# Kernel tuning notes

Hardware: AMD Instinct MI355X
Metric: run time of the kernel (lower is better)

The kernel has to match this reference:

```python
import jax, jax.numpy as jnp
import numpy as np


def setup_inputs() -> dict:
    key = jax.random.key(0)
    N, D = 131072, 128
    x = jax.random.normal(key, (N, D), dtype=jnp.float32)
    return {"x": x, "k": 1024, "niters": 10}


def reference(x, k, niters):
    """Lloyd's k-means, Euclidean metric. Returns (clusters, centroids, n_points).

    Matches torch semantics: clusters are the assignments computed at the START
    of the last iteration (against the previous centroids); centroids/n_points
    reflect the update performed in that last iteration. Empty clusters divide
    by zero (-> inf/nan), same as the torch code.
    """
    K = int(k)
    x_sq = jnp.sum(x * x, axis=-1)  # [N], constant across iterations
    c0 = x[:K]

    def step(centroids, _):
        d = (x_sq[:, None]
             - 2.0 * jnp.einsum('nd,kd->nk', x, centroids)
             + jnp.sum(centroids * centroids, axis=-1)[None, :])
        clusters = jnp.argmin(d, axis=1)  # [N] int32
        sums = jax.ops.segment_sum(x, clusters, num_segments=K)  # [K, D] scatter-add
        counts = jax.ops.segment_sum(jnp.ones((x.shape[0],), x.dtype), clusters,
                                     num_segments=K)  # [K] bincount
        new_centroids = sums / counts[:, None]
        return new_centroids, (clusters, counts)

    centroids, (clusters_hist, counts_hist) = jax.lax.scan(step, c0, None, length=int(niters))
    return clusters_hist[-1].astype(jnp.int64), centroids, counts_hist[-1]
```

## Files before the change

### kernel.cpp

```cpp
#include <hip/hip_runtime.h>
#include <math.h>

#define DIM 128
#define KC 1024
#define NITER 10
#define BM 128
#define NB 512
#define THRESH 0.01f

typedef __bf16 bf16x8 __attribute__((ext_vector_type(8)));
typedef float f32x4 __attribute__((ext_vector_type(4)));

__device__ __forceinline__ unsigned short bf16rne(float f) {
    unsigned int u = __float_as_uint(f);
    unsigned int r = (u + 0x7FFFu + ((u >> 16) & 1u)) >> 16;
    return (unsigned short)r;
}

__device__ __forceinline__ bf16x8 pack_hi8(const float* fv, unsigned short* hs) {
    bf16x8 out;
    #pragma unroll
    for (int e = 0; e < 8; e++) {
        unsigned short h = bf16rne(fv[e]);
        hs[e] = h;
        out[e] = __builtin_bit_cast(__bf16, h);
    }
    return out;
}

__device__ __forceinline__ float sq_np_row(const float* __restrict__ v) {
    const float4* row = (const float4*)v;
    float r[8];
    {
        float4 a = row[0], b = row[1];
        r[0] = __fmul_rn(a.x, a.x); r[1] = __fmul_rn(a.y, a.y);
        r[2] = __fmul_rn(a.z, a.z); r[3] = __fmul_rn(a.w, a.w);
        r[4] = __fmul_rn(b.x, b.x); r[5] = __fmul_rn(b.y, b.y);
        r[6] = __fmul_rn(b.z, b.z); r[7] = __fmul_rn(b.w, b.w);
    }
    #pragma unroll
    for (int blk = 1; blk < 16; blk++) {
        float4 a = row[blk * 2], b = row[blk * 2 + 1];
        r[0] = __fadd_rn(r[0], __fmul_rn(a.x, a.x));
        r[1] = __fadd_rn(r[1], __fmul_rn(a.y, a.y));
        r[2] = __fadd_rn(r[2], __fmul_rn(a.z, a.z));
        r[3] = __fadd_rn(r[3], __fmul_rn(a.w, a.w));
        r[4] = __fadd_rn(r[4], __fmul_rn(b.x, b.x));
        r[5] = __fadd_rn(r[5], __fmul_rn(b.y, b.y));
        r[6] = __fadd_rn(r[6], __fmul_rn(b.z, b.z));
        r[7] = __fadd_rn(r[7], __fmul_rn(b.w, b.w));
    }
    return __fadd_rn(__fadd_rn(__fadd_rn(r[0], r[1]), __fadd_rn(r[2], r[3])),
                     __fadd_rn(__fadd_rn(r[4], r[5]), __fadd_rn(r[6], r[7])));
}

__global__ void sq_np_kernel(const float* __restrict__ v, float* __restrict__ out, int rows) {
    int i = blockIdx.x * blockDim.x + threadIdx.x;
    if (i >= rows) return;
    out[i] = sq_np_row(v + (size_t)i * DIM);
}

__global__ __launch_bounds__(256, 3) void assign_mfma_kernel(
    const float* __restrict__ x,
    const ushort* __restrict__ centPh, const ushort* __restrict__ centPl,
    const float* __restrict__ csq,
    int* __restrict__ cl, int* __restrict__ fb_list, int* __restrict__ fbc)
{
    const int tid = threadIdx.x;
    const int lane = tid & 63;
    const int w = tid >> 6;
    const int bm = blockIdx.x * BM;
    const int row0 = bm + w * 32 + (lane & 15);
    const int ko = (lane >> 4) * 8;

    bf16x8 ah[2][4], al[2][4];
    #pragma unroll
    for (int m = 0; m < 2; m++) {
        const float* xr = x + (size_t)(row0 + m * 16) * DIM;
        #pragma unroll
        for (int dt = 0; dt < 4; dt++) {
            float4 a = *(const float4*)(xr + dt * 32 + ko);
            float4 b = *(const float4*)(xr + dt * 32 + ko + 4);
            float fv[8] = {a.x, a.y, a.z, a.w, b.x, b.y, b.z, b.w};
            unsigned short hs[8];
            ah[m][dt] = pack_hi8(fv, hs);
            bf16x8 lo;
            #pragma unroll
            for (int e = 0; e < 8; e++) {
                float rem = __fsub_rn(fv[e], __uint_as_float(((unsigned int)hs[e]) << 16));
                lo[e] = __builtin_bit_cast(__bf16, bf16rne(rem));
            }
            al[m][dt] = lo;
        }
    }

    float best1[8], best2[8];
    int bidx[8];
    int nanf = 0;
    #pragma unroll
    for (int s = 0; s < 8; s++) { best1[s] = INFINITY; best2[s] = INFINITY; bidx[s] = 0; }

    const ushort* pb = centPh + lane * 8;
    const ushort* qb = centPl + lane * 8;
    int kk = lane & 15;

    for (int kt = 0; kt < KC / 16; kt++) {
        const ushort* pk = pb + (size_t)kt * 2048;
        const ushort* qk = qb + (size_t)kt * 2048;
        bf16x8 bh0 = *(const bf16x8*)(pk);
        bf16x8 bh1 = *(const bf16x8*)(pk + 512);
        bf16x8 bh2 = *(const bf16x8*)(pk + 1024);
        bf16x8 bh3 = *(const bf16x8*)(pk + 1536);
        bf16x8 bl0 = *(const bf16x8*)(qk);
        bf16x8 bl1 = *(const bf16x8*)(qk + 512);
        bf16x8 bl2 = *(const bf16x8*)(qk + 1024);
        bf16x8 bl3 = *(const bf16x8*)(qk + 1536);

        f32x4 a0 = (f32x4){0.f, 0.f, 0.f, 0.f};
        f32x4 a1 = (f32x4){0.f, 0.f, 0.f, 0.f};
#define DT(BH, BL, D)                                                      \
        a0 = __builtin_amdgcn_mfma_f32_16x16x32_bf16(ah[0][D], BH, a0, 0, 0, 0); \
        a1 = __builtin_amdgcn_mfma_f32_16x16x32_bf16(ah[1][D], BH, a1, 0, 0, 0); \
        a0 = __builtin_amdgcn_mfma_f32_16x16x32_bf16(ah[0][D], BL, a0, 0, 0, 0); \
        a1 = __builtin_amdgcn_mfma_f32_16x16x32_bf16(ah[1][D], BL, a1, 0, 0, 0); \
        a0 = __builtin_amdgcn_mfma_f32_16x16x32_bf16(al[0][D], BH, a0, 0, 0, 0); \
        a1 = __builtin_amdgcn_mfma_f32_16x16x32_bf16(al[1][D], BH, a1, 0, 0, 0);
        DT(bh0, bl0, 0)
        DT(bh1, bl1, 1)
        DT(bh2, bl2, 2)
        DT(bh3, bl3, 3)
#undef DT

        float cq = csq[kk];
        nanf |= (cq != cq) ? 1 : 0;
        #pragma unroll
        for (int q = 0; q < 4; q++) {
            {
                float d = __fmaf_rn(-2.f, a0[q], cq);
                bool lt = (d < best1[q]);
                best2[q] = fminf(best2[q], lt ? best1[q] : d);
                if (lt) { best1[q] = d; bidx[q] = kk; }
            }
            {
                int s = 4 + q;
                float d = __fmaf_rn(-2.f, a1[q], cq);
                bool lt = (d < best1[s]);
                best2[s] = fminf(best2[s], lt ? best1[s] : d);
                if (lt) { best1[s] = d; bidx[s] = kk; }
            }
        }
        kk += 16;
    }

    #pragma unroll
    for (int mask = 1; mask < 16; mask <<= 1) {
        #pragma unroll
        for (int s = 0; s < 8; s++) {
            float ob1 = __shfl_xor(best1[s], mask, 64);
            float ob2 = __shfl_xor(best2[s], mask, 64);
            int   oi  = __shfl_xor(bidx[s],  mask, 64);
            float nb2 = fminf(fminf(best2[s], ob2), fmaxf(best1[s], ob1));
            bool take = (ob1 < best1[s]) || (ob1 == best1[s] && oi < bidx[s]);
            if (take) { best1[s] = ob1; bidx[s] = oi; }
            best2[s] = nb2;
        }
    }

    int wnan = __any(nanf);
    if ((lane & 15) == 0) {
        int hi = lane >> 4;
        #pragma unroll
        for (int s = 0; s < 8; s++) {
            int p = bm + w * 32 + (s >> 2) * 16 + hi * 4 + (s & 3);
            bool fb = (wnan != 0) || !(best2[s] - best1[s] > THRESH);
            if (fb) { int pos = atomicAdd(fbc, 1); fb_list[pos] = p; }
            else cl[p] = bidx[s];
        }
    }
}

__device__ __forceinline__ bool better(float od, int oi, float md, int mi) {
    bool n1 = (md != md), n2 = (od != od);
    if (n1 && n2) return oi < mi;
    if (n2) return true;
    if (n1) return false;
    return (od < md) || (od == md && oi < mi);
}

__global__ __launch_bounds__(256) void fixup_kernel(
    const float* __restrict__ x, const float* __restrict__ centTf,
    const float* __restrict__ xsq, const float* __restrict__ csq,
    const int* __restrict__ fb_list, const int* __restrict__ fbc,
    int* __restrict__ cl)
{
    __shared__ float xs[16][DIM];
    __shared__ float xqs[16];
    __shared__ int   ids[16];
    __shared__ float wv[16][4];
    __shared__ int   wi[16][4];
    const int t = threadIdx.x;
    const int lane = t & 63, wid = t >> 6;
    const int cnt = fbc[0];
    for (int w = blockIdx.x * 16; w < cnt; w += gridDim.x * 16) {
        int np = cnt - w; if (np > 16) np = 16;
        __syncthreads();
        if (t < np) { int i = fb_list[w + t]; ids[t] = i; xqs[t] = xsq[i]; }
        __syncthreads();
        for (int e = t; e < np * DIM; e += 256) {
            int p = e >> 7, d = e & 127;
            xs[p][d] = x[(size_t)ids[p] * DIM + d];
        }
        __syncthreads();
        float S[16][4];
        #pragma unroll
        for (int p = 0; p < 16; p++)
            #pragma unroll
            for (int c = 0; c < 4; c++) S[p][c] = 0.f;
        #pragma unroll 4
        for (int d = 0; d < DIM; d++) {
            const float* row = centTf + (size_t)d * KC;
            float c0 = row[t], c1 = row[t + 256], c2 = row[t + 512], c3 = row[t + 768];
            #pragma unroll
            for (int p = 0; p < 16; p++) {
                float xv = xs[p][d];
                S[p][0] = fmaf(xv, c0, S[p][0]);
                S[p][1] = fmaf(xv, c1, S[p][1]);
                S[p][2] = fmaf(xv, c2, S[p][2]);
                S[p][3] = fmaf(xv, c3, S[p][3]);
            }
        }
        float q0 = csq[t], q1 = csq[t + 256], q2 = csq[t + 512], q3 = csq[t + 768];
        #pragma unroll
        for (int p = 0; p < 16; p++) {
            float xq = xqs[p];
            float bb = INFINITY; int bi = 0x7fffffff;
            float dd; int c;
            c = t;       dd = __fadd_rn(__fsub_rn(xq, __fmul_rn(2.f, S[p][0])), q0); if (better(dd, c, bb, bi)) { bb = dd; bi = c; }
            c = t + 256; dd = __fadd_rn(__fsub_rn(xq, __fmul_rn(2.f, S[p][1])), q1); if (better(dd, c, bb, bi)) { bb = dd; bi = c; }
            c = t + 512; dd = __fadd_rn(__fsub_rn(xq, __fmul_rn(2.f, S[p][2])), q2); if (better(dd, c, bb, bi)) { bb = dd; bi = c; }
            c = t + 768; dd = __fadd_rn(__fsub_rn(xq, __fmul_rn(2.f, S[p][3])), q3); if (better(dd, c, bb, bi)) { bb = dd; bi = c; }
            #pragma unroll
            for (int mask = 1; mask < 64; mask <<= 1) {
                float od = __shfl_xor(bb, mask, 64);
                int   oi = __shfl_xor(bi, mask, 64);
                if (better(od, oi, bb, bi)) { bb = od; bi = oi; }
            }
            if (lane == 0) { wv[p][wid] = bb; wi[p][wid] = bi; }
        }
        __syncthreads();
        if (t < np) {
            float bb = wv[t][0]; int bi = wi[t][0];
            #pragma unroll
            for (int r = 1; r < 4; r++)
                if (better(wv[t][r], wi[t][r], bb, bi)) { bb = wv[t][r]; bi = wi[t][r]; }
            cl[ids[t]] = bi;
        }
    }
}


__global__ __launch_bounds__(256) void bhist_kernel(const int* __restrict__ cl,
                                                    int* __restrict__ bhist, int n,
                                                    int* __restrict__ fbc) {
    __shared__ int h[KC];
    int t = threadIdx.x;
    if (blockIdx.x == 0 && t == 0) { fbc[0] = 0; fbc[1] = 0; }
    #pragma unroll
    for (int q = 0; q < KC / 256; q++) h[t + q * 256] = 0;
    __syncthreads();
    int i = blockIdx.x * 256 + t;
    if (i < n) atomicAdd(&h[cl[i]], 1);
    __syncthreads();
    int* row = bhist + (size_t)blockIdx.x * KC;
    #pragma unroll
    for (int q = 0; q < KC / 256; q++) row[t + q * 256] = h[t + q * 256];
}

__global__ __launch_bounds__(256) void colsum_kernel(const int* __restrict__ bhist,
                                                     int* __restrict__ cnt) {
    int k = blockIdx.x * 256 + threadIdx.x;
    int s = 0;
    #pragma unroll 8
    for (int b = 0; b < NB; b++) s += bhist[(size_t)b * KC + k];
    cnt[k] = s;
}

__global__ __launch_bounds__(256) void blockpfx_kernel(int* __restrict__ bhist,
                                                       const int* __restrict__ cnt,
                                                       int* __restrict__ off) {
    __shared__ int lc[KC];
    __shared__ int ps[256];
    int t = threadIdx.x;
    int4 cv = *(const int4*)(cnt + t * 4);
    *(int4*)(lc + t * 4) = cv;
    ps[t] = cv.x + cv.y + cv.z + cv.w;
    __syncthreads();
    for (int o = 1; o < 256; o <<= 1) {
        int v = (t >= o) ? ps[t - o] : 0;
        __syncthreads();
        ps[t] += v;
        __syncthreads();
    }
    int k = blockIdx.x * 256 + t;
    int g = k >> 2;
    int run = (g > 0) ? ps[g - 1] : 0;
    for (int j = g * 4; j < k; j++) run += lc[j];
    off[k] = run;
    for (int b0 = 0; b0 < NB; b0 += 16) {
        int v[16];
        #pragma unroll
        for (int u = 0; u < 16; u++)
            v[u] = bhist[(size_t)(b0 + u) * KC + k];
        #pragma unroll
        for (int u = 0; u < 16; u++) {
            bhist[(size_t)(b0 + u) * KC + k] = run;
            run += v[u];
        }
    }
}

__global__ __launch_bounds__(256) void stable_scatter_kernel(
    const int* __restrict__ cl, const int* __restrict__ bhist,
    int* __restrict__ list, int n)
{
    __shared__ int cls[256];
    int t = threadIdx.x;
    int i = blockIdx.x * 256 + t;
    int c = (i < n) ? cl[i] : -1;
    cls[t] = c;
    __syncthreads();
    if (i >= n) return;
    int rank = 0;
    for (int j = 0; j < 256; j++)
        rank += (j < t && cls[j] == c) ? 1 : 0;
    list[bhist[(size_t)blockIdx.x * KC + c] + rank] = i;
}

#define CHUNK 512
__global__ __launch_bounds__(128) void sum_kernel(
    const float* __restrict__ x, const int* __restrict__ list,
    const int* __restrict__ off, const int* __restrict__ cnt,
    float* __restrict__ cent, ushort* __restrict__ centPh,
    ushort* __restrict__ centPl, float* __restrict__ centTf,
    float* __restrict__ csq, float* __restrict__ countsF)
{
    __attribute__((aligned(16))) __shared__ int sidx[CHUNK];
    int k = blockIdx.x;
    int d = threadIdx.x;
    int o = off[k], m = cnt[k];
    float s = 0.f;
    for (int base = 0; base < m; base += CHUNK) {
        int c = m - base; if (c > CHUNK) c = CHUNK;
        __syncthreads();
        for (int t = d; t < c; t += 128) sidx[t] = list[o + base + t];
        __syncthreads();
        int j = 0;
        for (; j + 16 <= c; j += 16) {
            float v[16];
            #pragma unroll
            for (int u = 0; u < 16; u++)
                v[u] = x[(size_t)sidx[j + u] * DIM + d];
            #pragma unroll
            for (int u = 0; u < 16; u++)
                s = __fadd_rn(s, v[u]);
        }
        for (; j < c; j++)
            s = __fadd_rn(s, x[(size_t)sidx[j] * DIM + d]);
    }
    float mv = __fdiv_rn(s, (float)m);
    cent[(size_t)k * DIM + d] = mv;
    centTf[(size_t)d * KC + k] = mv;
    unsigned short h = bf16rne(mv);
    unsigned short lo = bf16rne(__fsub_rn(mv, __uint_as_float(((unsigned int)h) << 16)));
    int pidx = (((k >> 4) * 4 + (d >> 5)) * 64 + ((k & 15) + 16 * ((d >> 3) & 3))) * 8 + (d & 7);
    centPh[pidx] = h;
    centPl[pidx] = lo;
    if (d == 0) countsF[k] = (float)m;
    __syncthreads();
    ((float*)sidx)[d] = mv;
    __syncthreads();
    if (d == 0) csq[k] = sq_np_row((const float*)sidx);
}

__global__ void init_centP_kernel(const float* __restrict__ x,
                                  ushort* __restrict__ centPh, ushort* __restrict__ centPl,
                                  float* __restrict__ centTf, int* __restrict__ fbc) {
    int i = blockIdx.x * 256 + threadIdx.x;
    if (i == 0) { fbc[0] = 0; fbc[1] = 0; }
    if (i < KC * DIM) {
        int k = i >> 7, d = i & 127;
        float v = x[i];
        centTf[(size_t)d * KC + k] = v;
        unsigned short h = bf16rne(v);
        unsigned short lo = bf16rne(__fsub_rn(v, __uint_as_float(((unsigned int)h) << 16)));
        int pidx = (((k >> 4) * 4 + (d >> 5)) * 64 + ((k & 15) + 16 * ((d >> 3) & 3))) * 8 + (d & 7);
        centPh[pidx] = h;
        centPl[pidx] = lo;
    }
}

__global__ void cl2f_kernel(const int* __restrict__ cl, float* __restrict__ out, int n) {
    int i = blockIdx.x * 256 + threadIdx.x;
    if (i < n) out[i] = (float)cl[i];
}

extern "C" void kernel_launch(void* const* d_in, const int* in_sizes, int n_in,
                              void* d_out, int out_size, void* d_ws, size_t ws_size,
                              hipStream_t stream) {
    const float* x = (const float*)d_in[0];
    const int n = in_sizes[0] / DIM;

    float* clf     = (float*)d_out;
    float* cent    = clf + n;
    float* countsF = cent + KC * DIM;

    float* xsq   = (float*)d_ws;
    float* csq   = xsq + n;
    int*   cl    = (int*)(csq + KC);
    int*   list  = cl + n;
    int*   cnt   = list + n;
    int*   off   = cnt + KC;
    int*   bhist = off + KC;
    ushort* centPh = (ushort*)(bhist + (size_t)NB * KC);
    ushort* centPl = centPh + KC * DIM;
    int*   fbc   = (int*)(centPl + KC * DIM);
    float* centTf = (float*)bhist;

    hipMemcpyAsync(cent, x, (size_t)KC * DIM * sizeof(float),
                   hipMemcpyDeviceToDevice, stream);
    init_centP_kernel<<<(KC * DIM + 255) / 256, 256, 0, stream>>>(x, centPh, centPl,
                                                                  centTf, fbc);
    sq_np_kernel<<<(n + 255) / 256, 256, 0, stream>>>(x, xsq, n);
    hipMemcpyAsync(csq, xsq, (size_t)KC * sizeof(float),
                   hipMemcpyDeviceToDevice, stream);

    for (int it = 0; it < NITER; it++) {
        assign_mfma_kernel<<<n / BM, 256, 0, stream>>>(x, centPh, centPl, csq,
                                                       cl, list, fbc);
        fixup_kernel<<<1024, 256, 0, stream>>>(x, centTf, xsq, csq, list, fbc, cl);
        bhist_kernel<<<NB, 256, 0, stream>>>(cl, bhist, n, fbc);
        colsum_kernel<<<KC / 256, 256, 0, stream>>>(bhist, cnt);
        blockpfx_kernel<<<KC / 256, 256, 0, stream>>>(bhist, cnt, off);
        stable_scatter_kernel<<<NB, 256, 0, stream>>>(cl, bhist, list, n);
        sum_kernel<<<KC, DIM, 0, stream>>>(x, list, off, cnt, cent, centPh, centPl,
                                           centTf, csq, countsF);
    }

    cl2f_kernel<<<(n + 255) / 256, 256, 0, stream>>>(cl, clf, n);
}
```

Before: 2.224 ms.

## Split centroid range across waves in assign kernel, merge top-2 via LDS

The assign kernel now gives each block 32 rows instead of 128. Its four waves each scan a quarter of the centroids for the same rows, and the per-wave best and second-best values are merged through shared memory. Occupancy is raised to 6 blocks per CU in launch bounds. This cuts per-wave serial loop length and raises parallelism, but each x row is converted to bf16 four times, centroid reads from L2 grow fourfold per row, and a block barrier is added. The NaN check now covers the whole block rather than a single wave.

```diff
diff --git a/kernel.cpp b/kernel.cpp
--- a/kernel.cpp
+++ b/kernel.cpp
@@ -4,7 +4,6 @@
 #define DIM 128
 #define KC 1024
 #define NITER 10
-#define BM 128
 #define NB 512
 #define THRESH 0.01f
 
@@ -60,17 +59,21 @@
     out[i] = sq_np_row(v + (size_t)i * DIM);
 }
 
-__global__ __launch_bounds__(256, 3) void assign_mfma_kernel(
+__global__ __launch_bounds__(256, 6) void assign_mfma_kernel(
     const float* __restrict__ x,
     const ushort* __restrict__ centPh, const ushort* __restrict__ centPl,
     const float* __restrict__ csq,
     int* __restrict__ cl, int* __restrict__ fb_list, int* __restrict__ fbc)
 {
+    __shared__ float sb1[4][32];
+    __shared__ float sb2[4][32];
+    __shared__ int   sidw[4][32];
+
     const int tid = threadIdx.x;
     const int lane = tid & 63;
-    const int w = tid >> 6;
-    const int bm = blockIdx.x * BM;
-    const int row0 = bm + w * 32 + (lane & 15);
+    const int wn = tid >> 6;
+    const int bm = blockIdx.x * 32;
+    const int row0 = bm + (lane & 15);
     const int ko = (lane >> 4) * 8;
 
     bf16x8 ah[2][4], al[2][4];
@@ -102,9 +105,8 @@
 
     const ushort* pb = centPh + lane * 8;
     const ushort* qb = centPl + lane * 8;
-    int kk = lane & 15;
-
-    for (int kt = 0; kt < KC / 16; kt++) {
+
+    for (int kt = wn * 16; kt < wn * 16 + 16; kt++) {
         const ushort* pk = pb + (size_t)kt * 2048;
         const ushort* qk = qb + (size_t)kt * 2048;
         bf16x8 bh0 = *(const bf16x8*)(pk);
@@ -131,6 +133,7 @@
         DT(bh3, bl3, 3)
 #undef DT
 
+        int kk = kt * 16 + (lane & 15);
         float cq = csq[kk];
         nanf |= (cq != cq) ? 1 : 0;
         #pragma unroll
@@ -149,7 +152,6 @@
                 if (lt) { best1[s] = d; bidx[s] = kk; }
             }
         }
-        kk += 16;
     }
 
     #pragma unroll
@@ -166,16 +168,30 @@
         }
     }
 
-    int wnan = __any(nanf);
     if ((lane & 15) == 0) {
         int hi = lane >> 4;
         #pragma unroll
         for (int s = 0; s < 8; s++) {
-            int p = bm + w * 32 + (s >> 2) * 16 + hi * 4 + (s & 3);
-            bool fb = (wnan != 0) || !(best2[s] - best1[s] > THRESH);
-            if (fb) { int pos = atomicAdd(fbc, 1); fb_list[pos] = p; }
-            else cl[p] = bidx[s];
-        }
+            int pl = (s >> 2) * 16 + hi * 4 + (s & 3);
+            sb1[wn][pl] = best1[s];
+            sb2[wn][pl] = best2[s];
+            sidw[wn][pl] = bidx[s];
+        }
+    }
+    int nanblk = __syncthreads_or(nanf);
+    if (tid < 32) {
+        float m1 = sb1[0][tid], m2 = sb2[0][tid];
+        int mi = sidw[0][tid];
+        #pragma unroll
+        for (int r = 1; r < 4; r++) {
+            float c1 = sb1[r][tid], c2 = sb2[r][tid];
+            int ci = sidw[r][tid];
+            m2 = fminf(fminf(m2, c2), fmaxf(m1, c1));
+            if (c1 < m1 || (c1 == m1 && ci < mi)) { m1 = c1; mi = ci; }
+        }
+        bool fb = (nanblk != 0) || !(m2 - m1 > THRESH);
+        if (fb) { int pos = atomicAdd(fbc, 1); fb_list[pos] = bm + tid; }
+        else cl[bm + tid] = mi;
     }
 }
 
@@ -435,7 +451,7 @@
                    hipMemcpyDeviceToDevice, stream);
 
     for (int it = 0; it < NITER; it++) {
-        assign_mfma_kernel<<<n / BM, 256, 0, stream>>>(x, centPh, centPl, csq,
+        assign_mfma_kernel<<<n / 32, 256, 0, stream>>>(x, centPh, centPl, csq,
                                                        cl, list, fbc);
         fixup_kernel<<<1024, 256, 0, stream>>>(x, centTf, xsq, csq, list, fbc, cl);
         bhist_kernel<<<NB, 256, 0, stream>>>(cl, bhist, n, fbc);
```

Result: slower. 5.415 ms (+143.5%).
